# Kernel optimization log

Measured on AMD Instinct MI355X. Metric: run time of the kernel, lower is better.

Reference implementation:

```python
import jax, jax.numpy as jnp
import numpy as np
import math

B, S, D, H, PD = 2, 2048, 1024, 16, 3
DK = D // H          # 64
SP = S // H          # 128, required so physics_scores matches scores shape


def setup_inputs() -> dict:
    key = jax.random.key(0)
    ks = jax.random.split(key, 16)
    sc = 0.02
    return {
        "query": jax.random.normal(ks[0], (B, S, D), jnp.float32),
        "key_in": jax.random.normal(ks[1], (B, S, D), jnp.float32),
        "value": jax.random.normal(ks[2], (B, S, D), jnp.float32),
        "physics_info": jax.random.normal(ks[3], (B, SP, PD), jnp.float32),
        "Wq": jax.random.normal(ks[4], (D, D), jnp.float32) * sc,
        "bq": jnp.zeros((D,), jnp.float32),
        "Wk": jax.random.normal(ks[5], (D, D), jnp.float32) * sc,
        "bk": jnp.zeros((D,), jnp.float32),
        "Wv": jax.random.normal(ks[6], (D, D), jnp.float32) * sc,
        "bv": jnp.zeros((D,), jnp.float32),
        "Wo": jax.random.normal(ks[7], (D, D), jnp.float32) * sc,
        "bo": jnp.zeros((D,), jnp.float32),
        "Pw": jax.random.normal(ks[8], (PD, D), jnp.float32),   # physics_weight
        "pb": jnp.zeros((1,), jnp.float32),                      # physics_bias
    }


def reference(query, key_in, value, physics_info, Wq, bq, Wk, bk, Wv, bv, Wo, bo, Pw, pb):
    b, s, d = query.shape
    inv = 1.0 / math.sqrt(DK)
    # project and split heads -> [B, H, S, DK]
    Q = (query @ Wq + bq).reshape(b, s, H, DK).transpose(0, 2, 1, 3)
    K = (key_in @ Wk + bk).reshape(b, s, H, DK).transpose(0, 2, 1, 3)
    V = (value @ Wv + bv).reshape(b, s, H, DK).transpose(0, 2, 1, 3)
    scores = jnp.einsum('bhqd,bhkd->bhqk', Q, K) * inv  # [B,H,S,S]
    # physics constraint: [B,SP,D] -> (expand over heads is a no-op) -> [B,SP*H,DK]
    pc = (physics_info @ Pw).reshape(b, SP * H, DK)
    physics_scores = jnp.einsum('bhqd,bkd->bhqk', Q, pc) * inv  # [B,H,S,S]
    scores = scores + pb[0] * physics_scores
    attn = jax.nn.softmax(scores, axis=-1)  # dropout in eval mode (identity)
    ctx = jnp.einsum('bhqk,bhkd->bhqd', attn, V)
    ctx = ctx.transpose(0, 2, 1, 3).reshape(b, s, d)
    return ctx @ Wo + bo
```

## Files before the change

kernel.cpp:

```cpp
#include <hip/hip_runtime.h>
#include <hip/hip_bf16.h>
#include <stdint.h>
#include <math.h>

typedef __bf16 bf16_t;
typedef __attribute__((ext_vector_type(8))) __bf16 bf16x8;
typedef __attribute__((ext_vector_type(4))) __bf16 bf16x4;
typedef __attribute__((ext_vector_type(4))) short short4_t;
typedef __attribute__((ext_vector_type(4))) float f32x4;

#define GLOBAL_AS(p) ((const __attribute__((address_space(1))) void*)(p))
#define LDS_AS(p)    ((__attribute__((address_space(3))) void*)(p))

#define B_ 2
#define S_ 2048
#define D_ 1024
#define H_ 16
#define DK_ 64
#define SP_ 128

#define QSCALE 0.1803368801111144f

static __device__ inline float fast_exp2(float x) {
#if __has_builtin(__builtin_amdgcn_exp2f)
    return __builtin_amdgcn_exp2f(x);
#else
    return __expf(x * 0.6931471805599453f);
#endif
}

static __device__ inline f32x4 mfma16x16x16bf16(short4_t a, short4_t b, f32x4 c) {
#if __has_builtin(__builtin_amdgcn_mfma_f32_16x16x16bf16_1k)
    return __builtin_amdgcn_mfma_f32_16x16x16bf16_1k(a, b, c, 0, 0, 0);
#else
    asm volatile("v_mfma_f32_16x16x16_bf16 %0, %1, %2, %0" : "+v"(c) : "v"(a), "v"(b));
    return c;
#endif
}

struct WPtrs { const float* w[4]; bf16_t* o[4]; };

__global__ __launch_bounds__(256) void prep(
    const float* __restrict__ q, const float* __restrict__ k,
    const float* __restrict__ v,
    bf16_t* __restrict__ qo, bf16_t* __restrict__ ko, bf16_t* __restrict__ vo,
    WPtrs wp, const float* __restrict__ phys, const float* __restrict__ Pw,
    float* __restrict__ PP) {
    int bx = blockIdx.x, tid = threadIdx.x;
    if (bx < 6144) {
        int z = bx >> 11, blk = bx & 2047;
        const float* in = (z == 0) ? q : (z == 1) ? k : v;
        bf16_t* out = (z == 0) ? qo : (z == 1) ? ko : vo;
        size_t i = ((size_t)blk * 256 + tid) * 8;
        f32x4 a = *(const f32x4*)(in + i);
        f32x4 b = *(const f32x4*)(in + i + 4);
        bf16x8 o;
#pragma unroll
        for (int e = 0; e < 4; ++e) { o[e] = (bf16_t)a[e]; o[4 + e] = (bf16_t)b[e]; }
        *(bf16x8*)(out + i) = o;
    } else if (bx < 10240) {
        __shared__ bf16_t t[32][33];
        int idx = bx - 6144;
        int z = idx >> 10;
        const float* W = wp.w[z];
        bf16_t* Wt = wp.o[z];
        int gx = (idx & 31) * 32, gy = ((idx >> 5) & 31) * 32;
        int x = tid & 31, y0 = tid >> 5;
#pragma unroll
        for (int j = 0; j < 32; j += 8)
            t[y0 + j][x] = (bf16_t)W[(size_t)(gy + y0 + j) * D_ + gx + x];
        __syncthreads();
#pragma unroll
        for (int j = 0; j < 32; j += 8)
            Wt[(size_t)(gx + y0 + j) * D_ + gy + x] = t[x][y0 + j];
    } else {
        int i = (bx - 10240) * 256 + tid;
        int n = i & (D_ - 1);
        int sb = i >> 10;
        float acc = 0.f;
#pragma unroll
        for (int p = 0; p < 3; ++p)
            acc += phys[sb * 3 + p] * Pw[p * D_ + n];
        PP[i] = acc;
    }
}

__global__ __launch_bounds__(256) void qkv_gemm(
    const bf16_t* __restrict__ Qi, const bf16_t* __restrict__ Ki,
    const bf16_t* __restrict__ Vi,
    const bf16_t* __restrict__ WqT, const bf16_t* __restrict__ WkT,
    const bf16_t* __restrict__ WvT,
    const float* __restrict__ bq, const float* __restrict__ bk,
    const float* __restrict__ bv,
    bf16_t* __restrict__ Qo, bf16_t* __restrict__ Ko, bf16_t* __restrict__ Vo,
    const float* __restrict__ PP, const float* __restrict__ pbp) {
    __shared__ alignas(16) bf16_t lA[128 * 64];
    __shared__ alignas(16) bf16_t lB[128 * 64];
    int z = blockIdx.z;
    const bf16_t* A = (z == 0) ? Qi : (z == 1) ? Ki : Vi;
    const bf16_t* Bt = (z == 0) ? WqT : (z == 1) ? WkT : WvT;
    const float* bias = (z == 0) ? bq : (z == 1) ? bk : bv;

    int tid = threadIdx.x;
    int lane = tid & 63, wid = tid >> 6;
    int quad = lane >> 4, l15 = lane & 15;
    int bm = blockIdx.x * 128;
    int bn = blockIdx.y * 128;
    int wm = (wid >> 1) * 64, wn = (wid & 1) * 64;
    f32x4 acc[4][4] = {};

    for (int k0 = 0; k0 < D_; k0 += 64) {
        __syncthreads();
        const char* gA = (const char*)(A + (size_t)bm * D_ + k0);
        const char* gB = (const char*)(Bt + (size_t)bn * D_ + k0);
#pragma unroll
        for (int j = 0; j < 4; ++j) {
            int woff = j * 4096 + wid * 1024;
            int fl = woff + lane * 16;
            int row = fl >> 7, col = fl & 127;
            __builtin_amdgcn_global_load_lds(GLOBAL_AS(gA + (size_t)row * (D_ * 2) + col),
                                             LDS_AS((char*)lA + woff), 16, 0, 0);
            __builtin_amdgcn_global_load_lds(GLOBAL_AS(gB + (size_t)row * (D_ * 2) + col),
                                             LDS_AS((char*)lB + woff), 16, 0, 0);
        }
        __syncthreads();
#pragma unroll
        for (int ks = 0; ks < 2; ++ks) {
            bf16x8 af[4], bfr[4];
#pragma unroll
            for (int i = 0; i < 4; ++i) {
                af[i] = *(const bf16x8*)((const char*)lA + (wm + i * 16 + l15) * 128 + ks * 64 + quad * 16);
                bfr[i] = *(const bf16x8*)((const char*)lB + (wn + i * 16 + l15) * 128 + ks * 64 + quad * 16);
            }
#pragma unroll
            for (int i = 0; i < 4; ++i)
#pragma unroll
                for (int j = 0; j < 4; ++j)
                    acc[i][j] = __builtin_amdgcn_mfma_f32_16x16x32_bf16(af[i], bfr[j], acc[i][j], 0, 0, 0);
        }
    }

    float pb0 = (z == 1) ? pbp[0] : 0.f;
#pragma unroll
    for (int i = 0; i < 4; ++i)
#pragma unroll
        for (int j = 0; j < 4; ++j) {
            int r0 = bm + wm + i * 16 + quad * 4;
            int c = bn + wn + j * 16 + l15;
            float bv_ = bias[c];
#pragma unroll
            for (int reg = 0; reg < 4; ++reg) {
                int r = r0 + reg;
                float v = acc[i][j][reg] + bv_;
                if (z == 0) {
                    Qo[(size_t)r * D_ + c] = (bf16_t)(v * QSCALE);
                } else if (z == 1) {
                    int b = r >> 11, s = r & (S_ - 1);
                    v += pb0 * PP[((size_t)(b * SP_ + (s >> 4)) << 10) + ((s & 15) << 6) + (c & 63)];
                    Ko[(size_t)r * D_ + c] = (bf16_t)v;
                } else {
                    int b = r >> 11, s = r & (S_ - 1);
                    Vo[(((size_t)b << 10) + c) * S_ + s] = (bf16_t)v;
                }
            }
        }
}

#define KSTR 144
#define VSTR 272

__global__ __launch_bounds__(256) void flash_attn(const bf16_t* Qb,
                                                  const bf16_t* __restrict__ Kb,
                                                  const bf16_t* __restrict__ Vt,
                                                  bf16_t* Ctx) {
    __shared__ alignas(16) char lK[128 * KSTR];
    __shared__ alignas(16) char lV[64 * VSTR];
    int tid = threadIdx.x, lane = tid & 63, wid = tid >> 6;
    int quad = lane >> 4, l15 = lane & 15;
    int q0 = blockIdx.x * 128;
    int h = blockIdx.y, b = blockIdx.z;
    const bf16_t* Qh = Qb + ((size_t)b * S_) * D_ + h * DK_;
    const bf16_t* Kh = Kb + ((size_t)b * S_) * D_ + h * DK_;
    const bf16_t* Vh = Vt + ((size_t)b * D_ + h * DK_) * S_;

    {
        const char* g = (const char*)(Qh + (size_t)q0 * D_);
#pragma unroll
        for (int j = 0; j < 4; ++j) {
            int flat = j * 4096 + tid * 16;
            bf16x8 v = *(const bf16x8*)(g + (size_t)(flat >> 7) * (D_ * 2) + (flat & 127));
            *(bf16x8*)(lK + (flat >> 7) * KSTR + (flat & 127)) = v;
        }
    }
    __syncthreads();
    bf16x8 qf[2][2];
#pragma unroll
    for (int mt = 0; mt < 2; ++mt)
#pragma unroll
        for (int ks = 0; ks < 2; ++ks)
            qf[mt][ks] = *(const bf16x8*)(lK + (wid * 32 + mt * 16 + l15) * KSTR + ks * 64 + quad * 16);

    f32x4 ot[4][2] = {};
    float l_i[2] = {0.f, 0.f};

    for (int t = 0; t < S_ / 128; ++t) {
        const char* gK = (const char*)(Kh + (size_t)t * 128 * D_);
        const char* gV = (const char*)(Vh + (size_t)t * 128);
        bf16x8 vk[4], vv[4];
#pragma unroll
        for (int j = 0; j < 4; ++j) {
            int flat = j * 4096 + tid * 16;
            vk[j] = *(const bf16x8*)(gK + (size_t)(flat >> 7) * (D_ * 2) + (flat & 127));
            vv[j] = *(const bf16x8*)(gV + (size_t)(flat >> 8) * (S_ * 2) + (flat & 255));
        }
        __syncthreads();
#pragma unroll
        for (int j = 0; j < 4; ++j) {
            int flat = j * 4096 + tid * 16;
            *(bf16x8*)(lK + (flat >> 7) * KSTR + (flat & 127)) = vk[j];
            *(bf16x8*)(lV + (flat >> 8) * VSTR + (flat & 255)) = vv[j];
        }
        __syncthreads();

        f32x4 sc[8][2];
#pragma unroll
        for (int kt = 0; kt < 8; ++kt)
#pragma unroll
            for (int mt = 0; mt < 2; ++mt) sc[kt][mt] = (f32x4){0.f, 0.f, 0.f, 0.f};
#pragma unroll
        for (int kt = 0; kt < 8; ++kt) {
            bf16x8 kf0 = *(const bf16x8*)(lK + (kt * 16 + l15) * KSTR + quad * 16);
            bf16x8 kf1 = *(const bf16x8*)(lK + (kt * 16 + l15) * KSTR + 64 + quad * 16);
#pragma unroll
            for (int mt = 0; mt < 2; ++mt) {
                sc[kt][mt] = __builtin_amdgcn_mfma_f32_16x16x32_bf16(kf0, qf[mt][0], sc[kt][mt], 0, 0, 0);
                sc[kt][mt] = __builtin_amdgcn_mfma_f32_16x16x32_bf16(kf1, qf[mt][1], sc[kt][mt], 0, 0, 0);
            }
        }

#pragma unroll
        for (int mt = 0; mt < 2; ++mt) {
            float rsum = 0.f;
#pragma unroll
            for (int kt = 0; kt < 8; ++kt)
#pragma unroll
                for (int r = 0; r < 4; ++r) {
                    float p = fast_exp2(sc[kt][mt][r]);
                    sc[kt][mt][r] = p;
                    rsum += p;
                }
            rsum += __shfl_xor(rsum, 16, 64);
            rsum += __shfl_xor(rsum, 32, 64);
            l_i[mt] += rsum;
        }

#pragma unroll
        for (int kt = 0; kt < 8; ++kt) {
            short4_t bp[2];
#pragma unroll
            for (int mt = 0; mt < 2; ++mt) {
                bf16x4 t4;
#pragma unroll
                for (int r = 0; r < 4; ++r) t4[r] = (bf16_t)sc[kt][mt][r];
                bp[mt] = *(short4_t*)&t4;
            }
#pragma unroll
            for (int dt = 0; dt < 4; ++dt) {
                bf16x4 a4 = *(const bf16x4*)(lV + (dt * 16 + l15) * VSTR + kt * 32 + quad * 8);
                short4_t ap = *(short4_t*)&a4;
#pragma unroll
                for (int mt = 0; mt < 2; ++mt)
                    ot[dt][mt] = mfma16x16x16bf16(ap, bp[mt], ot[dt][mt]);
            }
        }
    }

    __syncthreads();
#pragma unroll
    for (int mt = 0; mt < 2; ++mt) {
        float inv_l = 1.0f / l_i[mt];
#pragma unroll
        for (int dt = 0; dt < 4; ++dt) {
            bf16x4 t4;
#pragma unroll
            for (int r = 0; r < 4; ++r) t4[r] = (bf16_t)(ot[dt][mt][r] * inv_l);
            *(bf16x4*)(lK + (wid * 32 + mt * 16 + l15) * KSTR + dt * 32 + quad * 8) = t4;
        }
    }
    __syncthreads();
    {
        char* gout = (char*)(Ctx + ((size_t)b * S_ + q0) * D_ + h * DK_);
#pragma unroll
        for (int j = 0; j < 4; ++j) {
            int flat = j * 4096 + tid * 16;
            bf16x8 v = *(const bf16x8*)(lK + (flat >> 7) * KSTR + (flat & 127));
            *(bf16x8*)(gout + (size_t)(flat >> 7) * (D_ * 2) + (flat & 127)) = v;
        }
    }
}

__global__ __launch_bounds__(256) void gemm_out(const bf16_t* __restrict__ A,
                                                const bf16_t* __restrict__ Bt,
                                                const float* __restrict__ bias,
                                                float* __restrict__ C) {
    __shared__ alignas(16) bf16_t lA[128 * 64];
    __shared__ alignas(16) bf16_t lB[128 * 64];
    int tid = threadIdx.x;
    int lane = tid & 63, wid = tid >> 6;
    int quad = lane >> 4, l15 = lane & 15;
    int bm = blockIdx.x * 128;
    int bn = blockIdx.y * 128;
    int wm = (wid >> 1) * 64, wn = (wid & 1) * 64;
    f32x4 acc[4][4] = {};

    for (int k0 = 0; k0 < D_; k0 += 64) {
        __syncthreads();
        const char* gA = (const char*)(A + (size_t)bm * D_ + k0);
        const char* gB = (const char*)(Bt + (size_t)bn * D_ + k0);
#pragma unroll
        for (int j = 0; j < 4; ++j) {
            int woff = j * 4096 + wid * 1024;
            int fl = woff + lane * 16;
            int row = fl >> 7, col = fl & 127;
            __builtin_amdgcn_global_load_lds(GLOBAL_AS(gA + (size_t)row * (D_ * 2) + col),
                                             LDS_AS((char*)lA + woff), 16, 0, 0);
            __builtin_amdgcn_global_load_lds(GLOBAL_AS(gB + (size_t)row * (D_ * 2) + col),
                                             LDS_AS((char*)lB + woff), 16, 0, 0);
        }
        __syncthreads();
#pragma unroll
        for (int ks = 0; ks < 2; ++ks) {
            bf16x8 af[4], bfr[4];
#pragma unroll
            for (int i = 0; i < 4; ++i) {
                af[i] = *(const bf16x8*)((const char*)lA + (wm + i * 16 + l15) * 128 + ks * 64 + quad * 16);
                bfr[i] = *(const bf16x8*)((const char*)lB + (wn + i * 16 + l15) * 128 + ks * 64 + quad * 16);
            }
#pragma unroll
            for (int i = 0; i < 4; ++i)
#pragma unroll
                for (int j = 0; j < 4; ++j)
                    acc[i][j] = __builtin_amdgcn_mfma_f32_16x16x32_bf16(af[i], bfr[j], acc[i][j], 0, 0, 0);
        }
    }
#pragma unroll
    for (int i = 0; i < 4; ++i)
#pragma unroll
        for (int j = 0; j < 4; ++j) {
            int r0 = bm + wm + i * 16 + quad * 4;
            int c = bn + wn + j * 16 + l15;
            float bv_ = bias[c];
#pragma unroll
            for (int reg = 0; reg < 4; ++reg)
                C[(size_t)(r0 + reg) * D_ + c] = acc[i][j][reg] + bv_;
        }
}

extern "C" void kernel_launch(void* const* d_in, const int* in_sizes, int n_in,
                              void* d_out, int out_size, void* d_ws, size_t ws_size,
                              hipStream_t stream) {
    const float* query  = (const float*)d_in[0];
    const float* key_in = (const float*)d_in[1];
    const float* value  = (const float*)d_in[2];
    const float* phys   = (const float*)d_in[3];
    const float* Wq     = (const float*)d_in[4];
    const float* bq     = (const float*)d_in[5];
    const float* Wk     = (const float*)d_in[6];
    const float* bk     = (const float*)d_in[7];
    const float* Wv     = (const float*)d_in[8];
    const float* bv     = (const float*)d_in[9];
    const float* Wo     = (const float*)d_in[10];
    const float* bo     = (const float*)d_in[11];
    const float* Pw     = (const float*)d_in[12];
    const float* pb     = (const float*)d_in[13];

    char* ws = (char*)d_ws;
    const size_t MB = 1ull << 20;
    bf16_t* Kb  = (bf16_t*)(ws + 0 * MB);
    bf16_t* QC  = (bf16_t*)(ws + 8 * MB);
    bf16_t* Kin = (bf16_t*)(ws + 16 * MB);
    bf16_t* Vin = (bf16_t*)(ws + 24 * MB);
    bf16_t* WqT = (bf16_t*)(ws + 32 * MB);
    bf16_t* WkT = (bf16_t*)(ws + 34 * MB);
    bf16_t* WvT = (bf16_t*)(ws + 36 * MB);
    bf16_t* WoT = (bf16_t*)(ws + 38 * MB);
    float*  PP  = (float*)(ws + 40 * MB);
    bf16_t* Vt  = (bf16_t*)d_out;
    bf16_t* Qin = (bf16_t*)((char*)d_out + 8 * MB);

    WPtrs wp;
    wp.w[0] = Wq; wp.w[1] = Wk; wp.w[2] = Wv; wp.w[3] = Wo;
    wp.o[0] = WqT; wp.o[1] = WkT; wp.o[2] = WvT; wp.o[3] = WoT;

    prep<<<11264, 256, 0, stream>>>(query, key_in, value, Qin, Kin, Vin,
                                    wp, phys, Pw, PP);

    dim3 gq(32, 8, 3);
    qkv_gemm<<<gq, 256, 0, stream>>>(Qin, Kin, Vin, WqT, WkT, WvT,
                                     bq, bk, bv, QC, Kb, Vt, PP, pb);

    dim3 fg(S_ / 128, H_, B_);
    flash_attn<<<fg, 256, 0, stream>>>(QC, Kb, Vt, QC);

    dim3 gg(32, 8);
    gemm_out<<<gg, 256, 0, stream>>>(QC, WoT, bo, (float*)d_out);
}
```

Baseline: 253.7 us.

## Rewrite QKV GEMM with 256x256 tiles and 4-stage async LDS pipeline

Replaces the 128x128, 256-thread QKV projection GEMM with a 256x256-tile, 512-thread kernel that uses a 4-buffer LDS ring. Global-to-LDS loads are issued three k-steps ahead, and fine-grained vmcnt waits replace the double __syncthreads. The aim is to hide global memory latency and raise per-block data reuse. The cost is a large LDS footprint (128KB) and only 192 blocks, which may underfill the GPU's CUs and limit occupancy.

```diff
diff --git a/kernel.cpp b/kernel.cpp
--- a/kernel.cpp
+++ b/kernel.cpp
@@ -85,7 +85,12 @@
     }
 }
 
-__global__ __launch_bounds__(256) void qkv_gemm(
+#define GATE(N) do { \
+    asm volatile("s_waitcnt vmcnt(" #N ") lgkmcnt(0)" ::: "memory"); \
+    __builtin_amdgcn_s_barrier(); \
+    __builtin_amdgcn_sched_barrier(0); } while (0)
+
+__global__ __launch_bounds__(512, 2) void qkv_gemm8(
     const bf16_t* __restrict__ Qi, const bf16_t* __restrict__ Ki,
     const bf16_t* __restrict__ Vi,
     const bf16_t* __restrict__ WqT, const bf16_t* __restrict__ WkT,
@@ -94,8 +99,7 @@
     const float* __restrict__ bv,
     bf16_t* __restrict__ Qo, bf16_t* __restrict__ Ko, bf16_t* __restrict__ Vo,
     const float* __restrict__ PP, const float* __restrict__ pbp) {
-    __shared__ alignas(16) bf16_t lA[128 * 64];
-    __shared__ alignas(16) bf16_t lB[128 * 64];
+    __shared__ alignas(16) char lds[131072];
     int z = blockIdx.z;
     const bf16_t* A = (z == 0) ? Qi : (z == 1) ? Ki : Vi;
     const bf16_t* Bt = (z == 0) ? WqT : (z == 1) ? WkT : WvT;
@@ -104,45 +108,57 @@
     int tid = threadIdx.x;
     int lane = tid & 63, wid = tid >> 6;
     int quad = lane >> 4, l15 = lane & 15;
-    int bm = blockIdx.x * 128;
-    int bn = blockIdx.y * 128;
-    int wm = (wid >> 1) * 64, wn = (wid & 1) * 64;
-    f32x4 acc[4][4] = {};
-
-    for (int k0 = 0; k0 < D_; k0 += 64) {
-        __syncthreads();
-        const char* gA = (const char*)(A + (size_t)bm * D_ + k0);
-        const char* gB = (const char*)(Bt + (size_t)bn * D_ + k0);
-#pragma unroll
-        for (int j = 0; j < 4; ++j) {
-            int woff = j * 4096 + wid * 1024;
-            int fl = woff + lane * 16;
-            int row = fl >> 7, col = fl & 127;
-            __builtin_amdgcn_global_load_lds(GLOBAL_AS(gA + (size_t)row * (D_ * 2) + col),
-                                             LDS_AS((char*)lA + woff), 16, 0, 0);
-            __builtin_amdgcn_global_load_lds(GLOBAL_AS(gB + (size_t)row * (D_ * 2) + col),
-                                             LDS_AS((char*)lB + woff), 16, 0, 0);
-        }
-        __syncthreads();
-#pragma unroll
-        for (int ks = 0; ks < 2; ++ks) {
-            bf16x8 af[4], bfr[4];
-#pragma unroll
-            for (int i = 0; i < 4; ++i) {
-                af[i] = *(const bf16x8*)((const char*)lA + (wm + i * 16 + l15) * 128 + ks * 64 + quad * 16);
-                bfr[i] = *(const bf16x8*)((const char*)lB + (wn + i * 16 + l15) * 128 + ks * 64 + quad * 16);
-            }
-#pragma unroll
-            for (int i = 0; i < 4; ++i)
-#pragma unroll
-                for (int j = 0; j < 4; ++j)
-                    acc[i][j] = __builtin_amdgcn_mfma_f32_16x16x32_bf16(af[i], bfr[j], acc[i][j], 0, 0, 0);
-        }
+    int bm = blockIdx.x * 256;
+    int bn = blockIdx.y * 256;
+    int wm = (wid >> 2) * 128, wn = (wid & 3) * 64;
+    const char* gA = (const char*)(A + (size_t)bm * D_);
+    const char* gB = (const char*)(Bt + (size_t)bn * D_);
+    f32x4 acc[8][4] = {};
+
+    auto STAGE = [&](int t) {
+        char* dstA = lds + (t & 3) * 32768;
+        char* dstB = dstA + 16384;
+        const char* srcA = gA + t * 64;
+        const char* srcB = gB + t * 64;
+#pragma unroll
+        for (int r = 0; r < 2; ++r) {
+            int f = r * 8192 + tid * 16;
+            int row = f >> 6, col = f & 63;
+            __builtin_amdgcn_global_load_lds(GLOBAL_AS(srcA + (size_t)row * (D_ * 2) + col),
+                                             LDS_AS(dstA + f), 16, 0, 0);
+            __builtin_amdgcn_global_load_lds(GLOBAL_AS(srcB + (size_t)row * (D_ * 2) + col),
+                                             LDS_AS(dstB + f), 16, 0, 0);
+        }
+    };
+
+    STAGE(0); STAGE(1); STAGE(2);
+
+    for (int t = 0; t < 32; ++t) {
+        if (t < 30)       GATE(8);
+        else if (t == 30) GATE(4);
+        else              GATE(0);
+
+        if (t < 29) STAGE(t + 3);
+
+        const char* Ab = lds + (t & 3) * 32768;
+        const char* Bb = Ab + 16384;
+        bf16x8 af[8], bfr[4];
+#pragma unroll
+        for (int i = 0; i < 8; ++i)
+            af[i] = *(const bf16x8*)(Ab + (wm + i * 16 + l15) * 64 + quad * 16);
+#pragma unroll
+        for (int j = 0; j < 4; ++j)
+            bfr[j] = *(const bf16x8*)(Bb + (wn + j * 16 + l15) * 64 + quad * 16);
+#pragma unroll
+        for (int i = 0; i < 8; ++i)
+#pragma unroll
+            for (int j = 0; j < 4; ++j)
+                acc[i][j] = __builtin_amdgcn_mfma_f32_16x16x32_bf16(af[i], bfr[j], acc[i][j], 0, 0, 0);
     }
 
     float pb0 = (z == 1) ? pbp[0] : 0.f;
 #pragma unroll
-    for (int i = 0; i < 4; ++i)
+    for (int i = 0; i < 8; ++i)
 #pragma unroll
         for (int j = 0; j < 4; ++j) {
             int r0 = bm + wm + i * 16 + quad * 4;
@@ -395,9 +411,9 @@
     prep<<<11264, 256, 0, stream>>>(query, key_in, value, Qin, Kin, Vin,
                                     wp, phys, Pw, PP);
 
-    dim3 gq(32, 8, 3);
-    qkv_gemm<<<gq, 256, 0, stream>>>(Qin, Kin, Vin, WqT, WkT, WvT,
-                                     bq, bk, bv, QC, Kb, Vt, PP, pb);
+    dim3 gq(16, 4, 3);
+    qkv_gemm8<<<gq, 512, 0, stream>>>(Qin, Kin, Vin, WqT, WkT, WvT,
+                                      bq, bk, bv, QC, Kb, Vt, PP, pb);
 
     dim3 fg(S_ / 128, H_, B_);
     flash_attn<<<fg, 256, 0, stream>>>(QC, Kb, Vt, QC);
```

New measurement: 261.8 us. 1.03x slower.
